# Optimization experiments

Measured on AMD Instinct MI355X. Metric: run time of the kernel, lower is better.

Reference implementation:

```python
import jax, jax.numpy as jnp
import numpy as np

B, L, E, H = 2, 2048, 1024, 16
D = E // H

def setup_inputs() -> dict:
    key = jax.random.key(0)
    ks = jax.random.split(key, 6)
    s = 1.0 / np.sqrt(E)
    return {
        "x": jax.random.normal(ks[0], (B, L, E), dtype=jnp.float32),
        "attention_mask": jnp.ones((B, L), dtype=jnp.float32),
        "Wq": jax.random.normal(ks[1], (E, E), dtype=jnp.float32) * s,
        "Wk": jax.random.normal(ks[2], (E, E), dtype=jnp.float32) * s,
        "Wv": jax.random.normal(ks[3], (E, E), dtype=jnp.float32) * s,
        "Wo": jax.random.normal(ks[4], (E, E), dtype=jnp.float32) * s,
        "bo": jnp.zeros((E,), dtype=jnp.float32),
    }

def reference(x, attention_mask, Wq, Wk, Wv, Wo, bo):
    b, l, e = x.shape
    h, d = H, D

    def proj(W):
        # (B,L,E) @ (E,E)^T -> (B,L,E) -> (B,H,L,D)
        return (x @ W.T).reshape(b, l, h, d).transpose(0, 2, 1, 3)

    q, k, v = proj(Wq), proj(Wk), proj(Wv)

    # multiplicative attention mask on q, k, v (mask shape (B,L) -> (B,1,L,1))
    m = attention_mask[:, None, :, None].astype(x.dtype)
    q, k, v = q * m, k * m, v * m

    scale = 1.0 / np.sqrt(d)
    scores = jnp.einsum('bhqd,bhkd->bhqk', q, k) * scale  # (B,H,L,L)
    causal = jnp.tril(jnp.ones((l, l), dtype=bool))
    scores = jnp.where(causal[None, None], scores, -jnp.inf)
    attn = jax.nn.softmax(scores, axis=-1)
    y = jnp.einsum('bhqk,bhkd->bhqd', attn, v)  # (B,H,L,D)
    y = y.transpose(0, 2, 1, 3).reshape(b, l, e)
    return y @ Wo.T + bo
```

## Files before the change

kernel.cpp:

```cpp
#include <hip/hip_runtime.h>
#include <cstdint>
#include <cstddef>
#include <math.h>

#define BB 2
#define LL 2048
#define EE 1024
#define HH 16
#define DD 64
#define MM (BB*LL)

typedef short short8 __attribute__((ext_vector_type(8)));
typedef float f32x4 __attribute__((ext_vector_type(4)));
typedef float f32x16 __attribute__((ext_vector_type(16)));

#define GPTR __attribute__((address_space(1)))
#define LPTR __attribute__((address_space(3)))

__device__ __forceinline__ unsigned short f32_bf16(float f) {
  union { float f; unsigned u; } c; c.f = f;
  c.u += 0x7fffu + ((c.u >> 16) & 1u);
  return (unsigned short)(c.u >> 16);
}

__device__ __forceinline__ unsigned pk_bf16(float lo, float hi) {
  unsigned r;
  asm("v_cvt_pk_bf16_f32 %0, %1, %2" : "=v"(r) : "v"(lo), "v"(hi));
  return r;
}
__device__ __forceinline__ void swap32(unsigned &a, unsigned &b) {
  asm("v_permlane32_swap_b32 %0, %1" : "+v"(a), "+v"(b));
}
__device__ __forceinline__ float xh_max(float v) {
  union { float f; unsigned u; } a, b;
  a.f = v;
  asm("v_mov_b32 %0, %1" : "=&v"(b.u) : "v"(a.u));
  asm("v_permlane32_swap_b32 %0, %1" : "+v"(a.u), "+v"(b.u));
  return fmaxf(a.f, b.f);
}
__device__ __forceinline__ float xh_sum(float v) {
  union { float f; unsigned u; } a, b;
  a.f = v;
  asm("v_mov_b32 %0, %1" : "=&v"(b.u) : "v"(a.u));
  asm("v_permlane32_swap_b32 %0, %1" : "+v"(a.u), "+v"(b.u));
  return a.f + b.f;
}
__device__ __forceinline__ f32x16 zero16() {
  f32x16 v;
  #pragma unroll
  for (int e = 0; e < 16; ++e) v[e] = 0.f;
  return v;
}

__global__ void cvt_all(const float* __restrict__ x,  const float* __restrict__ wq,
                        const float* __restrict__ wk, const float* __restrict__ wv,
                        const float* __restrict__ wo,
                        unsigned short* __restrict__ xb,  unsigned short* __restrict__ wqb,
                        unsigned short* __restrict__ wkb, unsigned short* __restrict__ wvb,
                        unsigned short* __restrict__ wob)
{
  int i = (blockIdx.x * 256 + threadIdx.x) * 4;
  if (i >= MM * EE + 4 * EE * EE) return;
  const float* s; unsigned short* d; int off;
  if (i < MM * EE) { s = x; d = xb; off = i; }
  else {
    int k = i - MM * EE;
    int w = k >> 20;
    off = k & (EE * EE - 1);
    s = (w == 0) ? wq : (w == 1) ? wk : (w == 2) ? wv : wo;
    d = (w == 0) ? wqb : (w == 1) ? wkb : (w == 2) ? wvb : wob;
  }
  float4 v = *(const float4*)(s + off);
  union { unsigned short s[4]; uint2 u; } o;
  o.s[0] = f32_bf16(v.x); o.s[1] = f32_bf16(v.y);
  o.s[2] = f32_bf16(v.z); o.s[3] = f32_bf16(v.w);
  *(uint2*)(d + off) = o.u;
}

template<int MODE>
__global__ __launch_bounds__(256, 2)
void gemm128(const unsigned short* __restrict__ A,
             const unsigned short* __restrict__ W0,
             const unsigned short* __restrict__ W1,
             const unsigned short* __restrict__ W2,
             const float* __restrict__ mask,
             const float* __restrict__ bias,
             unsigned short* __restrict__ O0,
             unsigned short* __restrict__ O1,
             unsigned short* __restrict__ O2,
             float* __restrict__ OF)
{
  constexpr int K = EE;
  const int tid = threadIdx.x;
  const int lane = tid & 63;
  const int wid = tid >> 6;
  const int g = lane >> 4, li = lane & 15;
  const int m0 = blockIdx.y * 128;
  const int n0 = blockIdx.x * 128;
  const int z = blockIdx.z;

  const unsigned short* Wp = W0;
  if (MODE == 0) Wp = (z == 0) ? W0 : ((z == 1) ? W1 : W2);

  __shared__ unsigned short As[128 * 64];
  __shared__ unsigned short Bs[128 * 64];

  f32x4 acc[4][4];
  f32x4 zero = {0.f, 0.f, 0.f, 0.f};
  #pragma unroll
  for (int i = 0; i < 4; ++i)
    #pragma unroll
    for (int j = 0; j < 4; ++j) acc[i][j] = zero;

  const int wm = (wid >> 1) * 64;
  const int wn = (wid & 1) * 64;

  for (int kt = 0; kt < K; kt += 64) {
    #pragma unroll
    for (int j = 0; j < 4; ++j) {
      int c = j * 256 + tid;
      int row = c >> 3;
      int lcol = ((c & 7) * 16) ^ ((row & 7) << 4);
      __builtin_amdgcn_global_load_lds(
        (const GPTR void*)((const char*)(A + (size_t)(m0 + row) * K + kt) + lcol),
        (LPTR void*)((char*)As + c * 16), 16, 0, 0);
      __builtin_amdgcn_global_load_lds(
        (const GPTR void*)((const char*)(Wp + (size_t)(n0 + row) * K + kt) + lcol),
        (LPTR void*)((char*)Bs + c * 16), 16, 0, 0);
    }
    __syncthreads();

    #pragma unroll
    for (int kk = 0; kk < 2; ++kk) {
      short8 a[4], b[4];
      const int colb = (kk * 32 + g * 8) * 2;
      #pragma unroll
      for (int i = 0; i < 4; ++i) {
        int ar = wm + i * 16 + li;
        a[i] = *(const short8*)((const char*)As + ar * 128 + (colb ^ ((ar & 7) << 4)));
        int br = wn + i * 16 + li;
        b[i] = *(const short8*)((const char*)Bs + br * 128 + (colb ^ ((br & 7) << 4)));
      }
      #pragma unroll
      for (int i = 0; i < 4; ++i)
        #pragma unroll
        for (int j = 0; j < 4; ++j)
          acc[i][j] = __builtin_amdgcn_mfma_f32_16x16x32_bf16(a[i], b[j], acc[i][j], 0, 0, 0);
    }
    __syncthreads();
  }

  if (MODE == 0) {
    if (z == 2) {
      #pragma unroll
      for (int i = 0; i < 4; ++i) {
        int mbase = m0 + wm + i * 16 + g * 4;
        int bb2 = mbase >> 11;
        int l0  = mbase & (LL - 1);
        float mk[4];
        #pragma unroll
        for (int r = 0; r < 4; ++r) mk[r] = mask[mbase + r];
        #pragma unroll
        for (int j = 0; j < 4; ++j) {
          int n = n0 + wn + j * 16 + li;
          int h2 = n >> 6, dd2 = n & 63;
          union { unsigned short s[4]; uint2 u; } o;
          #pragma unroll
          for (int r = 0; r < 4; ++r) o.s[r] = f32_bf16(acc[i][j][r] * mk[r]);
          size_t off = (size_t)(bb2 * HH + h2) * (LL * DD)
                     + (size_t)(l0 >> 5) * (DD * 32) + dd2 * 32 + (l0 & 31);
          *(uint2*)(O2 + off) = o.u;
        }
      }
    } else {
      unsigned short* Op = (z == 0) ? O0 : O1;
      const float sc = (z == 0) ? 0.125f * 1.44269504088896f : 1.0f;
      #pragma unroll
      for (int i = 0; i < 4; ++i) {
        #pragma unroll
        for (int r = 0; r < 4; ++r) {
          int m = m0 + wm + i * 16 + g * 4 + r;
          float mk = mask[m] * sc;
          int bb = m >> 11;
          int l  = m & (LL - 1);
          #pragma unroll
          for (int j = 0; j < 4; ++j) {
            int n = n0 + wn + j * 16 + li;
            int h = n >> 6, d = n & 63;
            size_t off = (((size_t)(bb * HH + h)) * LL + l) * DD + d;
            Op[off] = f32_bf16(acc[i][j][r] * mk);
          }
        }
      }
    }
  } else {
    #pragma unroll
    for (int i = 0; i < 4; ++i) {
      #pragma unroll
      for (int j = 0; j < 4; ++j) {
        int n = n0 + wn + j * 16 + li;
        float bv = bias[n];
        #pragma unroll
        for (int r = 0; r < 4; ++r) {
          int m = m0 + wm + i * 16 + g * 4 + r;
          OF[(size_t)m * EE + n] = acc[i][j][r] + bv;
        }
      }
    }
  }
}

__global__ __launch_bounds__(128, 2)
void attn5(const unsigned short* __restrict__ Q,
           const unsigned short* __restrict__ K,
           const unsigned short* __restrict__ VT,
           unsigned short* __restrict__ Y)
{
  const int tid = threadIdx.x, lane = tid & 63, w = tid >> 6;
  const int l31 = lane & 31, hi = lane >> 5;

  const int id = blockIdx.x;
  const int lo = id & 7;
  const int r_ = id >> 3;
  const int bh = (r_ & 3) * 8 + lo;
  const int p  = r_ >> 2;
  const int qth = 63 - p;
  const int qtl = p;
  const int b = bh >> 4, h = bh & (HH - 1);
  const size_t kbase = (size_t)bh * LL * DD;

  const unsigned short* Kg  = K + kbase;
  const unsigned short* VTg = VT + kbase;

  const int qrh = qth * 32 + l31;
  const int qrl = qtl * 32 + l31;

  short8 qfh[4], qfl[4];
  {
    const unsigned short* Qr = Q + kbase + (size_t)qrh * DD + hi * 8;
    #pragma unroll
    for (int kc = 0; kc < 4; ++kc) qfh[kc] = *(const short8*)(Qr + kc * 16);
    const unsigned short* Qs = Q + kbase + (size_t)qrl * DD + hi * 8;
    #pragma unroll
    for (int kc = 0; kc < 4; ++kc) qfl[kc] = *(const short8*)(Qs + kc * 16);
  }

  f32x16 oh0 = zero16(), oh1 = zero16(), ol0 = zero16(), ol1 = zero16();
  float mh = -INFINITY, lsh = 0.f, ml = -INFINITY, lsl = 0.f;

  short8 kA[4], vA[4], kB[4], vB[4];

  auto loadtile = [&](short8 (&kk)[4], short8 (&vv)[4], int t2) {
    const int kv0 = t2 << 5;
    const unsigned short* Kp = Kg + ((size_t)(kv0 + l31) << 6) + hi * 8;
    #pragma unroll
    for (int kc = 0; kc < 4; ++kc) kk[kc] = *(const short8*)(Kp + kc * 16);
    const unsigned short* Vp = VTg + (size_t)(kv0 >> 5) * (DD * 32) + l31 * 32 + hi * 8;
    vv[0] = *(const short8*)(Vp);
    vv[1] = *(const short8*)(Vp + 16);
    vv[2] = *(const short8*)(Vp + 32 * 32);
    vv[3] = *(const short8*)(Vp + 32 * 32 + 16);
  };

  loadtile(kA, vA, w);

  auto qk = [&](const short8 (&ck)[4], const short8 (&qf)[4]) -> f32x16 {
    f32x16 s = zero16();
    __builtin_amdgcn_s_setprio(1);
    #pragma unroll
    for (int kc = 0; kc < 4; ++kc)
      s = __builtin_amdgcn_mfma_f32_32x32x16_bf16(ck[kc], qf[kc], s, 0, 0, 0);
    __builtin_amdgcn_s_setprio(0);
    return s;
  };

  auto process = [&](f32x16 s, const short8 (&cv)[4],
                     float &mq, float &lq, f32x16 &o0, f32x16 &o1) {
    float red[8];
    #pragma unroll
    for (int e = 0; e < 8; ++e) red[e] = fmaxf(s[e], s[e + 8]);
    #pragma unroll
    for (int st = 4; st >= 1; st >>= 1)
      #pragma unroll
      for (int e = 0; e < 4; ++e) if (e < st) red[e] = fmaxf(red[e], red[e + st]);
    float mv = xh_max(red[0]);

    if (!__all(mv <= mq + 8.0f)) {
      float mnew = fmaxf(mq, mv);
      float al = exp2f(mq - mnew);
      mq = mnew;
      lq *= al;
      #pragma unroll
      for (int e = 0; e < 16; ++e) { o0[e] *= al; o1[e] *= al; }
    }

    float ra[8];
    #pragma unroll
    for (int e = 0; e < 16; ++e) s[e] = exp2f(s[e] - mq);
    #pragma unroll
    for (int e = 0; e < 8; ++e) ra[e] = s[e] + s[e + 8];
    #pragma unroll
    for (int st = 4; st >= 1; st >>= 1)
      #pragma unroll
      for (int e = 0; e < 4; ++e) if (e < st) ra[e] += ra[e + st];
    lq += xh_sum(ra[0]);

    auto mkfrag = [&](int base) -> short8 {
      unsigned a0 = pk_bf16(s[base + 0], s[base + 1]);
      unsigned a1 = pk_bf16(s[base + 2], s[base + 3]);
      unsigned b0 = pk_bf16(s[base + 4], s[base + 5]);
      unsigned b1 = pk_bf16(s[base + 6], s[base + 7]);
      swap32(a0, b0);
      swap32(a1, b1);
      union { unsigned u[4]; short8 s8; } f;
      f.u[0] = a0; f.u[1] = a1; f.u[2] = b0; f.u[3] = b1;
      return f.s8;
    };
    short8 pf0 = mkfrag(0), pf1 = mkfrag(8);

    __builtin_amdgcn_s_setprio(1);
    o0 = __builtin_amdgcn_mfma_f32_32x32x16_bf16(cv[0], pf0, o0, 0, 0, 0);
    o0 = __builtin_amdgcn_mfma_f32_32x32x16_bf16(cv[1], pf1, o0, 0, 0, 0);
    o1 = __builtin_amdgcn_mfma_f32_32x32x16_bf16(cv[2], pf0, o1, 0, 0, 0);
    o1 = __builtin_amdgcn_mfma_f32_32x32x16_bf16(cv[3], pf1, o1, 0, 0, 0);
    __builtin_amdgcn_s_setprio(0);
  };

  auto body = [&](short8 (&ck)[4], short8 (&cv)[4],
                  short8 (&nk)[4], short8 (&nv)[4], int t) {
    if (t + 2 <= qth) loadtile(nk, nv, t + 2);

    {
      f32x16 s = qk(ck, qfh);
      if (t == qth) {
        #pragma unroll
        for (int i = 0; i < 16; ++i) {
          int kvr = (i & 3) + 8 * (i >> 2) + 4 * hi;
          if (kvr > l31) s[i] = -INFINITY;
        }
      }
      process(s, cv, mh, lsh, oh0, oh1);
    }
    if (t <= qtl) {
      f32x16 s = qk(ck, qfl);
      if (t == qtl) {
        #pragma unroll
        for (int i = 0; i < 16; ++i) {
          int kvr = (i & 3) + 8 * (i >> 2) + 4 * hi;
          if (kvr > l31) s[i] = -INFINITY;
        }
      }
      process(s, cv, ml, lsl, ol0, ol1);
    }
  };

  for (int t = w; t <= qth; t += 4) {
    body(kA, vA, kB, vB, t);
    if (t + 2 <= qth) body(kB, vB, kA, vA, t + 2);
  }

  __shared__ float mg[2][64][34];
  if (w == 1) {
    mg[0][lane][0] = mh; mg[0][lane][1] = lsh;
    mg[1][lane][0] = ml; mg[1][lane][1] = lsl;
    #pragma unroll
    for (int e = 0; e < 16; ++e) {
      mg[0][lane][2 + e] = oh0[e]; mg[0][lane][18 + e] = oh1[e];
      mg[1][lane][2 + e] = ol0[e]; mg[1][lane][18 + e] = ol1[e];
    }
  }
  __syncthreads();
  if (w == 0) {
    #pragma unroll
    for (int q = 0; q < 2; ++q) {
      float mw = (q == 0) ? mh : ml;
      float lw = (q == 0) ? lsh : lsl;
      const f32x16& o0 = (q == 0) ? oh0 : ol0;
      const f32x16& o1 = (q == 0) ? oh1 : ol1;
      int qrow = (q == 0) ? qrh : qrl;
      float m1 = mg[q][lane][0], l1 = mg[q][lane][1];
      float M = fmaxf(mw, m1);
      float a0 = exp2f(mw - M), a1 = exp2f(m1 - M);
      float Lt = lw * a0 + l1 * a1;
      float inv = 1.0f / Lt;
      unsigned short* Yr = Y + ((size_t)b * LL + qrow) * EE + h * DD;
      #pragma unroll
      for (int rg = 0; rg < 4; ++rg) {
        union { unsigned short s[4]; uint2 u; } u0, u1;
        #pragma unroll
        for (int e = 0; e < 4; ++e) {
          int i = rg * 4 + e;
          u0.s[e] = f32_bf16((o0[i] * a0 + mg[q][lane][2 + i]  * a1) * inv);
          u1.s[e] = f32_bf16((o1[i] * a0 + mg[q][lane][18 + i] * a1) * inv);
        }
        *(uint2*)(Yr + rg * 8 + hi * 4) = u0.u;
        *(uint2*)(Yr + 32 + rg * 8 + hi * 4) = u1.u;
      }
    }
  }
}

extern "C" void kernel_launch(void* const* d_in, const int* in_sizes, int n_in,
                              void* d_out, int out_size, void* d_ws, size_t ws_size,
                              hipStream_t stream) {
  const float* x    = (const float*)d_in[0];
  const float* mask = (const float*)d_in[1];
  const float* Wq   = (const float*)d_in[2];
  const float* Wk   = (const float*)d_in[3];
  const float* Wv   = (const float*)d_in[4];
  const float* Wo   = (const float*)d_in[5];
  const float* bo   = (const float*)d_in[6];
  float* out = (float*)d_out;

  char* ws = (char*)d_ws;
  unsigned short* xb  = (unsigned short*)(ws);
  unsigned short* wqb = (unsigned short*)(ws + ((size_t)8  << 20));
  unsigned short* wkb = (unsigned short*)(ws + ((size_t)10 << 20));
  unsigned short* wvb = (unsigned short*)(ws + ((size_t)12 << 20));
  unsigned short* wob = (unsigned short*)(ws + ((size_t)14 << 20));
  unsigned short* Qb  = (unsigned short*)(ws + ((size_t)16 << 20));
  unsigned short* Kb  = (unsigned short*)(ws + ((size_t)24 << 20));
  unsigned short* VTb = (unsigned short*)(ws + ((size_t)32 << 20));
  unsigned short* Yb  = (unsigned short*)(ws + ((size_t)40 << 20));

  cvt_all<<<8192, 256, 0, stream>>>(x, Wq, Wk, Wv, Wo, xb, wqb, wkb, wvb, wob);

  gemm128<0><<<dim3(EE / 128, MM / 128, 3), 256, 0, stream>>>(
      xb, wqb, wkb, wvb, mask, nullptr, Qb, Kb, VTb, nullptr);

  attn5<<<dim3(1024), 128, 0, stream>>>(Qb, Kb, VTb, Yb);

  gemm128<1><<<dim3(EE / 128, MM / 128, 1), 256, 0, stream>>>(
      Yb, wob, nullptr, nullptr, nullptr, bo, nullptr, nullptr, nullptr, out);
}
```

Before: 111.1 us.

## Split attention KV loop across four waves with tree merge of softmax state

The attention kernel now runs with 256 threads (four waves) per block instead of two. The waves interleave KV tiles with stride 8 and prefetch four tiles ahead. Their online-softmax partial states are then merged through LDS in a two-level tree. The max reduction is also rewritten as a flatter expression. The intent is more parallelism per query tile, shortening the serial KV loop, at the cost of extra LDS, extra barriers and merge work, plus higher register pressure under the new launch bounds.

```diff
diff --git a/kernel.cpp b/kernel.cpp
--- a/kernel.cpp
+++ b/kernel.cpp
@@ -210,8 +210,8 @@
   }
 }
 
-__global__ __launch_bounds__(128, 2)
-void attn5(const unsigned short* __restrict__ Q,
+__global__ __launch_bounds__(256, 4)
+void attn6(const unsigned short* __restrict__ Q,
            const unsigned short* __restrict__ K,
            const unsigned short* __restrict__ VT,
            unsigned short* __restrict__ Y)
@@ -264,26 +264,21 @@
 
   loadtile(kA, vA, w);
 
-  auto qk = [&](const short8 (&ck)[4], const short8 (&qf)[4]) -> f32x16 {
-    f32x16 s = zero16();
+  auto qk = [&](const short8 (&ck)[4], const short8 (&qf)[4], f32x16 &sref) {
+    sref = zero16();
     __builtin_amdgcn_s_setprio(1);
     #pragma unroll
     for (int kc = 0; kc < 4; ++kc)
-      s = __builtin_amdgcn_mfma_f32_32x32x16_bf16(ck[kc], qf[kc], s, 0, 0, 0);
+      sref = __builtin_amdgcn_mfma_f32_32x32x16_bf16(ck[kc], qf[kc], sref, 0, 0, 0);
     __builtin_amdgcn_s_setprio(0);
-    return s;
-  };
-
-  auto process = [&](f32x16 s, const short8 (&cv)[4],
+  };
+
+  auto process = [&](f32x16 &s, const short8 (&cv)[4],
                      float &mq, float &lq, f32x16 &o0, f32x16 &o1) {
-    float red[8];
-    #pragma unroll
-    for (int e = 0; e < 8; ++e) red[e] = fmaxf(s[e], s[e + 8]);
-    #pragma unroll
-    for (int st = 4; st >= 1; st >>= 1)
-      #pragma unroll
-      for (int e = 0; e < 4; ++e) if (e < st) red[e] = fmaxf(red[e], red[e + st]);
-    float mv = xh_max(red[0]);
+    float r0 = fmaxf(fmaxf(fmaxf(s[0], s[8]),  fmaxf(s[1], s[9])),  fmaxf(s[2], s[10]));
+    float r1 = fmaxf(fmaxf(fmaxf(s[3], s[11]), fmaxf(s[4], s[12])), fmaxf(s[5], s[13]));
+    float r2 = fmaxf(fmaxf(s[6], s[14]), fmaxf(s[7], s[15]));
+    float mv = xh_max(fmaxf(fmaxf(r0, r1), r2));
 
     if (!__all(mv <= mq + 8.0f)) {
       float mnew = fmaxf(mq, mv);
@@ -328,10 +323,11 @@
 
   auto body = [&](short8 (&ck)[4], short8 (&cv)[4],
                   short8 (&nk)[4], short8 (&nv)[4], int t) {
-    if (t + 2 <= qth) loadtile(nk, nv, t + 2);
-
+    if (t + 4 <= qth) loadtile(nk, nv, t + 4);
+
+    f32x16 s;
     {
-      f32x16 s = qk(ck, qfh);
+      qk(ck, qfh, s);
       if (t == qth) {
         #pragma unroll
         for (int i = 0; i < 16; ++i) {
@@ -342,7 +338,7 @@
       process(s, cv, mh, lsh, oh0, oh1);
     }
     if (t <= qtl) {
-      f32x16 s = qk(ck, qfl);
+      qk(ck, qfl, s);
       if (t == qtl) {
         #pragma unroll
         for (int i = 0; i < 16; ++i) {
@@ -354,35 +350,54 @@
     }
   };
 
-  for (int t = w; t <= qth; t += 4) {
+  for (int t = w; t <= qth; t += 8) {
     body(kA, vA, kB, vB, t);
-    if (t + 2 <= qth) body(kB, vB, kA, vA, t + 2);
-  }
-
-  __shared__ float mg[2][64][34];
-  if (w == 1) {
-    mg[0][lane][0] = mh; mg[0][lane][1] = lsh;
-    mg[1][lane][0] = ml; mg[1][lane][1] = lsl;
+    if (t + 4 <= qth) body(kB, vB, kA, vA, t + 4);
+  }
+
+  __shared__ float mg[2][2][64][34];
+
+  auto storeState = [&](int s_) {
+    mg[s_][0][lane][0] = mh; mg[s_][0][lane][1] = lsh;
+    mg[s_][1][lane][0] = ml; mg[s_][1][lane][1] = lsl;
     #pragma unroll
     for (int e = 0; e < 16; ++e) {
-      mg[0][lane][2 + e] = oh0[e]; mg[0][lane][18 + e] = oh1[e];
-      mg[1][lane][2 + e] = ol0[e]; mg[1][lane][18 + e] = ol1[e];
-    }
-  }
+      mg[s_][0][lane][2 + e] = oh0[e]; mg[s_][0][lane][18 + e] = oh1[e];
+      mg[s_][1][lane][2 + e] = ol0[e]; mg[s_][1][lane][18 + e] = ol1[e];
+    }
+  };
+  auto mergeState = [&](int s_, int q, float &mq, float &lq, f32x16 &o0, f32x16 &o1) {
+    float m1 = mg[s_][q][lane][0], l1 = mg[s_][q][lane][1];
+    float M = fmaxf(mq, m1);
+    float a0 = exp2f(fmaxf(mq - M, -200.0f));
+    float a1 = exp2f(fmaxf(m1 - M, -200.0f));
+    lq = lq * a0 + l1 * a1;
+    mq = M;
+    #pragma unroll
+    for (int e = 0; e < 16; ++e) {
+      o0[e] = o0[e] * a0 + mg[s_][q][lane][2 + e]  * a1;
+      o1[e] = o1[e] * a0 + mg[s_][q][lane][18 + e] * a1;
+    }
+  };
+
+  if (w == 1) storeState(0);
+  if (w == 3) storeState(1);
+  __syncthreads();
+  if (w == 0) { mergeState(0, 0, mh, lsh, oh0, oh1); mergeState(0, 1, ml, lsl, ol0, ol1); }
+  if (w == 2) { mergeState(1, 0, mh, lsh, oh0, oh1); mergeState(1, 1, ml, lsl, ol0, ol1); }
+  __syncthreads();
+  if (w == 2) storeState(0);
   __syncthreads();
   if (w == 0) {
+    mergeState(0, 0, mh, lsh, oh0, oh1);
+    mergeState(0, 1, ml, lsl, ol0, ol1);
     #pragma unroll
     for (int q = 0; q < 2; ++q) {
-      float mw = (q == 0) ? mh : ml;
-      float lw = (q == 0) ? lsh : lsl;
+      float lq = (q == 0) ? lsh : lsl;
       const f32x16& o0 = (q == 0) ? oh0 : ol0;
       const f32x16& o1 = (q == 0) ? oh1 : ol1;
       int qrow = (q == 0) ? qrh : qrl;
-      float m1 = mg[q][lane][0], l1 = mg[q][lane][1];
-      float M = fmaxf(mw, m1);
-      float a0 = exp2f(mw - M), a1 = exp2f(m1 - M);
-      float Lt = lw * a0 + l1 * a1;
-      float inv = 1.0f / Lt;
+      float inv = 1.0f / lq;
       unsigned short* Yr = Y + ((size_t)b * LL + qrow) * EE + h * DD;
       #pragma unroll
       for (int rg = 0; rg < 4; ++rg) {
@@ -390,8 +405,8 @@
         #pragma unroll
         for (int e = 0; e < 4; ++e) {
           int i = rg * 4 + e;
-          u0.s[e] = f32_bf16((o0[i] * a0 + mg[q][lane][2 + i]  * a1) * inv);
-          u1.s[e] = f32_bf16((o1[i] * a0 + mg[q][lane][18 + i] * a1) * inv);
+          u0.s[e] = f32_bf16(o0[i] * inv);
+          u1.s[e] = f32_bf16(o1[i] * inv);
         }
         *(uint2*)(Yr + rg * 8 + hi * 4) = u0.u;
         *(uint2*)(Yr + 32 + rg * 8 + hi * 4) = u1.u;
@@ -428,7 +443,7 @@
   gemm128<0><<<dim3(EE / 128, MM / 128, 3), 256, 0, stream>>>(
       xb, wqb, wkb, wvb, mask, nullptr, Qb, Kb, VTb, nullptr);
 
-  attn5<<<dim3(1024), 128, 0, stream>>>(Qb, Kb, VTb, Yb);
+  attn6<<<dim3(1024), 256, 0, stream>>>(Qb, Kb, VTb, Yb);
 
   gemm128<1><<<dim3(EE / 128, MM / 128, 1), 256, 0, stream>>>(
       Yb, wob, nullptr, nullptr, nullptr, bo, nullptr, nullptr, nullptr, out);
```

Result: slower. 210.3 us (+89.3%).
